# Kernel optimization log

Measured on AMD Instinct MI355X. Metric: run time of the kernel, lower is better.

## Reference

```python
import jax, jax.numpy as jnp
import numpy as np

KNN_K = 5          # neighbor count hard-coded in the original forward (get_entropy(..., k=5))
SAMPLE_K = 256     # self.k: number of tokens sampled per batch item
EPS = 1e-12


def _knn_entropy(x):
    """Per-point k-NN entropy weight: distance to the KNN_K-th nearest neighbor.

    x: [B, N, D] -> [B, N] nonnegative weights (Kozachenko-Leonenko style; the
    per-point entropy contribution is monotone in log d_k, and multinomial
    weights must be nonnegative, so we use d_k itself as the weight).
    """
    B, N, D = x.shape
    sq = jnp.sum(x * x, axis=-1)                                   # [B, N]
    d2 = sq[:, :, None] + sq[:, None, :] - 2.0 * jnp.einsum('bnd,bmd->bnm', x, x)  # [B,N,N]
    d2 = jnp.maximum(d2, 0.0)
    idx = jnp.arange(N)
    d2 = d2.at[:, idx, idx].set(jnp.inf)                           # exclude self
    neg_smallest, _ = jax.lax.top_k(-d2, KNN_K)                    # [B, N, KNN_K]
    dk2 = -neg_smallest[..., -1]                                   # sq dist to k-th NN
    return jnp.sqrt(dk2 + EPS)                                     # [B, N]


def setup_inputs() -> dict:
    key = jax.random.key(0)
    x = jax.random.normal(key, (8, 4096, 256), dtype=jnp.float32)
    return {"x": x}


def reference(x):
    # entropy weights per token (batched; replaces the per-batch numpy loop)
    w = _knn_entropy(x)                                            # [B, N]
    # multinomial sampling WITHOUT replacement via Gumbel top-k trick
    key = jax.random.key(42)
    g = jax.random.gumbel(key, w.shape, dtype=w.dtype)             # [B, N]
    scores = jnp.log(w + EPS) + g
    _, sampled_idx = jax.lax.top_k(scores, SAMPLE_K)               # [B, SAMPLE_K]
    # gather sampled tokens
    sampled = jnp.take_along_axis(x, sampled_idx[:, :, None], axis=1)  # [B, SAMPLE_K, D]
    return (sampled, 0.0)
```

## Files before the change

### kernel.cpp

```cpp
#include <hip/hip_runtime.h>
#include <math.h>
#include <stdint.h>

#define BATCH 8
#define NTOK  4096
#define DIM   256
#define SK    256
#define BQ    128
#define BM    128
#define BK    64
#define MH    2048
#define TOPK  10
#define CANDH 44

typedef __attribute__((ext_vector_type(8))) _Float16 half8;
typedef __attribute__((ext_vector_type(4))) float float4v;
typedef __attribute__((ext_vector_type(16))) float f32x16;

#define GLOAD_LDS16(gp, lp)                                                    \
  __builtin_amdgcn_global_load_lds(                                            \
      (const __attribute__((address_space(1))) unsigned int*)(gp),             \
      (__attribute__((address_space(3))) unsigned int*)(lp), 16, 0, 0)

__device__ __forceinline__ uint32_t umin32(uint32_t a, uint32_t b) { return a < b ? a : b; }
__device__ __forceinline__ uint32_t umax32(uint32_t a, uint32_t b) { return a > b ? a : b; }

__device__ __forceinline__ uint32_t rotl32(uint32_t v, uint32_t r) {
  return (v << r) | (v >> (32u - r));
}
__device__ __forceinline__ void tf_round4(uint32_t& x0, uint32_t& x1,
                                          uint32_t r0, uint32_t r1,
                                          uint32_t r2, uint32_t r3) {
  x0 += x1; x1 = rotl32(x1, r0); x1 ^= x0;
  x0 += x1; x1 = rotl32(x1, r1); x1 ^= x0;
  x0 += x1; x1 = rotl32(x1, r2); x1 ^= x0;
  x0 += x1; x1 = rotl32(x1, r3); x1 ^= x0;
}
__device__ __forceinline__ uint32_t threefry_bits32(uint32_t c_hi, uint32_t c_lo) {
  const uint32_t k0 = 0u, k1 = 42u;
  const uint32_t k2 = k0 ^ k1 ^ 0x1BD11BDAu;
  uint32_t x0 = c_hi + k0;
  uint32_t x1 = c_lo + k1;
  tf_round4(x0, x1, 13u, 15u, 26u, 6u);  x0 += k1; x1 += k2 + 1u;
  tf_round4(x0, x1, 17u, 29u, 16u, 24u); x0 += k2; x1 += k0 + 2u;
  tf_round4(x0, x1, 13u, 15u, 26u, 6u);  x0 += k0; x1 += k1 + 3u;
  tf_round4(x0, x1, 17u, 29u, 16u, 24u); x0 += k1; x1 += k2 + 4u;
  tf_round4(x0, x1, 13u, 15u, 26u, 6u);  x0 += k2; x1 += k0 + 5u;
  return x0 ^ x1;
}

__global__ __launch_bounds__(256) void tofp16_rowsq_kernel(
    const float* __restrict__ x, unsigned short* __restrict__ xh,
    float* __restrict__ sqf) {
  const int row  = blockIdx.x * 4 + (threadIdx.x >> 6);
  const int lane = threadIdx.x & 63;
  const float* xr = x + (size_t)row * DIM;
  double acc = 0.0;
#pragma unroll
  for (int i = 0; i < 4; ++i) {
    const float v = xr[lane + i * 64];
    const _Float16 h = (_Float16)v;
    xh[(size_t)row * DIM + lane + i * 64] = *(const unsigned short*)&h;
    acc += (double)v * (double)v;
  }
#pragma unroll
  for (int off = 32; off > 0; off >>= 1) acc += __shfl_down(acc, off, 64);
  if (lane == 0) sqf[row] = (float)acc;
}

__global__ __launch_bounds__(256, 2) void gemm_knn_kernel(
    const unsigned short* __restrict__ xh, const float* __restrict__ sqf,
    int* __restrict__ cand) {
  __shared__ union {
    unsigned short Bf[2][8192];
    uint32_t M[512][TOPK];
  } U;

  const int wid = (blockIdx.x & 7) * 64 + (blockIdx.x >> 3);
  const int b   = wid >> 6;
  const int qt  = (wid >> 1) & 31;
  const int mh  = wid & 1;
  const int q0  = qt * BQ;
  const int mbase = mh * MH;
  const int t  = threadIdx.x;
  const int w  = t >> 6;
  const int l  = t & 63;
  const int l5 = l & 31;
  const int hi2 = l >> 5;

  const unsigned short* xhb = xh + (size_t)b * NTOK * DIM;
  const float* sqb = sqf + b * NTOK;

  auto stageB = [&](int buf, int m0s, int kb) {
    const int m = m0s + w * 32 + l5;
    const unsigned short* src = xhb + (size_t)m * DIM + kb + hi2 * 8;
#pragma unroll
    for (int c = 0; c < 4; ++c) {
      GLOAD_LDS16(src + c * 16,
                  (char*)&U.Bf[0][0] + buf * 16384 + (c * 4 + w) * 1024 + l * 16);
    }
  };
  stageB(0, mbase, 0);

  const int qg = q0 + w * 32 + l5;
  const unsigned short* qrow = xhb + (size_t)qg * DIM;
  half8 af[16];
#pragma unroll
  for (int kk = 0; kk < 16; ++kk)
    af[kk] = *(const half8*)(qrow + kk * 16 + hi2 * 8);
  const float sqq = sqb[qg];

  __syncthreads();

  uint32_t tv0[TOPK], tv1[TOPK];
#pragma unroll
  for (int j = 0; j < TOPK; ++j) { tv0[j] = 0xFFFFFFFFu; tv1[j] = 0xFFFFFFFFu; }

  for (int mt = 0; mt < MH / BM; ++mt) {
    const int m0 = mbase + mt * BM;
    f32x16 acc[4];
#pragma unroll
    for (int ii = 0; ii < 4; ++ii) acc[ii] = (f32x16)(0.0f);

#pragma unroll
    for (int ks = 0; ks < 4; ++ks) {
      const int s = mt * 4 + ks;
      const int buf = s & 1;
      if (s + 1 < (MH / BM) * 4) {
        const int sn = s + 1;
        stageB(buf ^ 1, mbase + (sn >> 2) * BM, (sn & 3) * BK);
      }
#pragma unroll
      for (int kap = 0; kap < 4; ++kap) {
        const int kk = ks * 4 + kap;
#pragma unroll
        for (int ii = 0; ii < 4; ++ii) {
          const half8 mf = *(const half8*)((const char*)&U.Bf[0][0] +
                                           buf * 16384 + (kap * 4 + ii) * 1024 + l * 16);
          acc[ii] = __builtin_amdgcn_mfma_f32_32x32x16_f16(mf, af[kk], acc[ii], 0, 0, 0);
        }
      }
      __syncthreads();
    }

#pragma unroll
    for (int ii = 0; ii < 4; ++ii) {
      const int mb = m0 + ii * 32 + hi2 * 4;
#pragma unroll
      for (int c = 0; c < 4; ++c) {
        const float4v sqm = *(const float4v*)(sqb + mb + c * 8);
        uint32_t* tv = (c < 2) ? tv0 : tv1;
#pragma unroll
        for (int r = 0; r < 4; ++r) {
          const int mg = mb + c * 8 + r;
          const float d2a = sqq + sqm[r] - 2.0f * acc[ii][c * 4 + r];
          uint32_t v = (__float_as_uint(d2a) & 0xFFFFF000u) | (uint32_t)mg;
          if (v < tv[TOPK - 1]) {
            uint32_t vv = v;
#pragma unroll
            for (int k2 = 0; k2 < TOPK; ++k2) {
              const uint32_t lo = umin32(tv[k2], vv);
              vv = umax32(tv[k2], vv);
              tv[k2] = lo;
            }
          }
        }
      }
    }
  }

  __syncthreads();
  {
    const int base = ((w * 32 + l5) << 2) + (hi2 << 1);
#pragma unroll
    for (int j = 0; j < TOPK; ++j) { U.M[base][j] = tv0[j]; U.M[base + 1][j] = tv1[j]; }
  }
  __syncthreads();
  if (t < BQ) {
    const int q = t;
    const int qglob = q0 + q;
    const int kidx = ((qglob >> 11) == mh) ? 5 : 4;
    uint32_t t6[6];
#pragma unroll
    for (int j = 0; j < 6; ++j) t6[j] = 0xFFFFFFFFu;
    for (int s = 0; s < 4; ++s)
      for (int j = 0; j < 6; ++j) {
        const uint32_t v = U.M[q * 4 + s][j];
        if (v < t6[5]) {
          uint32_t vv = v;
#pragma unroll
          for (int k2 = 0; k2 < 6; ++k2) {
            const uint32_t lo = umin32(t6[k2], vv);
            vv = umax32(t6[k2], vv);
            t6[k2] = lo;
          }
        }
      }
    const float T = __uint_as_float(t6[kidx] & 0xFFFFF000u) + 2.0f;
    int cnt = 0, ov = 0;
    int* cq = cand + (size_t)(b * NTOK + qglob) * (2 * CANDH) + mh * CANDH;
    for (int s = 0; s < 4; ++s) {
      const uint32_t last = U.M[q * 4 + s][TOPK - 1];
      if (__uint_as_float(last & 0xFFFFF000u) < T) ov = 1;
      for (int j = 0; j < TOPK; ++j) {
        const uint32_t v = U.M[q * 4 + s][j];
        if (__uint_as_float(v & 0xFFFFF000u) <= T && cnt < 4 * TOPK)
          cq[1 + cnt++] = (int)(v & 0xFFFu);
      }
    }
    cq[0] = ov ? -1 : cnt;
  }
}

__global__ __launch_bounds__(256) void exact_knn_score_kernel(
    const float* __restrict__ x, const int* __restrict__ cand,
    double* __restrict__ scores) {
  const int qg = blockIdx.x * 4 + (threadIdx.x >> 6);
  const int l  = threadIdx.x & 63;
  const int b  = qg >> 12;
  const int q  = qg & (NTOK - 1);
  const float* xb = x + (size_t)b * NTOK * DIM;
  const int* cq = cand + (size_t)qg * (2 * CANDH);

  double xq[4];
#pragma unroll
  for (int i = 0; i < 4; ++i) xq[i] = (double)xb[(size_t)q * DIM + l + i * 64];

  double t5[5] = {1e300, 1e300, 1e300, 1e300, 1e300};
  auto ins5 = [&](double v) {
    if (v < t5[4]) {
      t5[4] = v;
#pragma unroll
      for (int k2 = 4; k2 > 0; --k2)
        if (t5[k2] < t5[k2 - 1]) { double tmp = t5[k2]; t5[k2] = t5[k2 - 1]; t5[k2 - 1] = tmp; }
    }
  };
  auto process = [&](int m) {
    double acc = 0.0;
#pragma unroll
    for (int i = 0; i < 4; ++i) {
      const double d = xq[i] - (double)xb[(size_t)m * DIM + l + i * 64];
      acc += d * d;
    }
#pragma unroll
    for (int off = 32; off > 0; off >>= 1) acc += __shfl_xor(acc, off, 64);
    ins5(acc);
  };

  for (int h = 0; h < 2; ++h) {
    const int cnt = cq[h * CANDH];
    if (cnt >= 0) {
      for (int c = 0; c < cnt; ++c) {
        const int m = cq[h * CANDH + 1 + c];
        if (m == q) continue;
        process(m);
      }
    } else {
      const int mb2 = h * MH;
      double mv[5] = {1e300, 1e300, 1e300, 1e300, 1e300};
      const float4v* qr4 = (const float4v*)(xb + (size_t)q * DIM);
      for (int it = 0; it < MH / 64; ++it) {
        const int m = mb2 + it * 64 + l;
        if (m == q) continue;
        const float4v* xr4 = (const float4v*)(xb + (size_t)m * DIM);
        double acc = 0.0;
#pragma unroll 16
        for (int d4 = 0; d4 < DIM / 4; ++d4) {
          const float4v qa = qr4[d4];
          const float4v xa = xr4[d4];
#pragma unroll
          for (int j = 0; j < 4; ++j) {
            const double df = (double)qa[j] - (double)xa[j];
            acc += df * df;
          }
        }
        if (acc < mv[4]) {
          mv[4] = acc;
#pragma unroll
          for (int k2 = 4; k2 > 0; --k2)
            if (mv[k2] < mv[k2 - 1]) { double tmp = mv[k2]; mv[k2] = mv[k2 - 1]; mv[k2 - 1] = tmp; }
        }
      }
      int p = 0;
#pragma unroll
      for (int r5 = 0; r5 < 5; ++r5) {
        double best = (p < 5) ? mv[p] : 1e300;
        double mn = best;
#pragma unroll
        for (int off = 32; off > 0; off >>= 1) {
          const double o = __shfl_xor(mn, off, 64);
          mn = (o < mn) ? o : mn;
        }
        const unsigned long long msk = __ballot(best == mn);
        if (l == (int)(__ffsll(msk) - 1)) ++p;
        ins5(mn);
      }
    }
  }

  if (l == 0) {
    const uint32_t bits = threefry_bits32(0u, (uint32_t)qg);
    const uint32_t fb = (bits >> 9) | 0x3F800000u;
    float uf = __uint_as_float(fb) - 1.0f;
    const float tiny = 1.17549435082228750797e-38f;
    uf += tiny;
    if (uf < tiny) uf = tiny;
    const double g = -log(-log((double)uf));
    const double wv = sqrt(t5[4] + 1e-12);
    scores[qg] = log(wv + 1e-12) + g;
  }
}

__global__ __launch_bounds__(1024) void sort_topk_kernel(
    const double* __restrict__ scores, int* __restrict__ sel) {
  __shared__ unsigned long long ko[NTOK];
  __shared__ int ki[NTOK];
  const int b = blockIdx.x;
  const int t = threadIdx.x;
  for (int i = t; i < NTOK; i += 1024) {
    const double s = scores[(size_t)b * NTOK + i];
    unsigned long long u = (unsigned long long)__double_as_longlong(s);
    u = (u & 0x8000000000000000ull) ? ~u : (u | 0x8000000000000000ull);
    ko[i] = u; ki[i] = i;
  }
  __syncthreads();
  for (int k = 2; k <= NTOK; k <<= 1) {
    for (int j = k >> 1; j > 0; j >>= 1) {
      for (int base = 0; base < NTOK; base += 1024) {
        const int i = base + t;
        const int p = i ^ j;
        if (p > i) {
          const bool up = (i & k) == 0;
          unsigned long long a = ko[i], c = ko[p];
          int ia = ki[i], ic = ki[p];
          const bool p_beats = (c > a) || (c == a && ic < ia);
          const bool i_beats = (a > c) || (a == c && ia < ic);
          const bool sw = up ? p_beats : i_beats;
          if (sw) { ko[i] = c; ko[p] = a; ki[i] = ic; ki[p] = ia; }
        }
      }
      __syncthreads();
    }
  }
  if (t < SK) sel[b * SK + t] = ki[t];
}

__global__ __launch_bounds__(256) void gather_kernel(const float* __restrict__ x,
                                                     const int* __restrict__ sel,
                                                     float* __restrict__ out) {
  const int blk = blockIdx.x;
  const int b = blk >> 8;
  const int r = blk & 255;
  const int t = threadIdx.x;
  const int src = sel[b * SK + r];
  out[((size_t)(b * SK + r)) * DIM + t] = x[((size_t)(b * NTOK + src)) * DIM + t];
  if (blk == 0 && t == 0) out[(size_t)BATCH * SK * DIM] = 0.0f;
}

extern "C" void kernel_launch(void* const* d_in, const int* in_sizes, int n_in,
                              void* d_out, int out_size, void* d_ws, size_t ws_size,
                              hipStream_t stream) {
  const float* x = (const float*)d_in[0];
  float* out = (float*)d_out;
  char* ws = (char*)d_ws;

  double* scores  = (double*)(ws + 0);
  float*  sqf     = (float*)(ws + 262144);
  int*    sel     = (int*)(ws + 393216);
  unsigned short* xh = (unsigned short*)(ws + 1048576);
  int*    cand    = (int*)(ws + 17825792);

  tofp16_rowsq_kernel<<<BATCH * NTOK / 4, 256, 0, stream>>>(x, xh, sqf);
  gemm_knn_kernel<<<BATCH * (NTOK / BQ) * 2, 256, 0, stream>>>(xh, sqf, cand);
  exact_knn_score_kernel<<<BATCH * NTOK / 4, 256, 0, stream>>>(x, cand, scores);
  sort_topk_kernel<<<BATCH, 1024, 0, stream>>>(scores, sel);
  gather_kernel<<<BATCH * SK, 256, 0, stream>>>(x, sel, out);
}
```

Measured before the change: 452.6 us.

## Switch kNN GEMM to 16x16x32 MFMA with 512-thread blocks

Rewrites the distance GEMM in the kNN kernel to use 16x16x32 f16 MFMA instructions with 8 waves per block instead of 32x32x16 with 4 waves. The K step per stage is doubled, so there are half as many barrier-separated stages, and the LDS buffers are doubled to hold it. Each lane now keeps a single top-10 list instead of two. The aim is more waves in flight and fewer syncs. The cost is double the LDS use per block and more MFMA instructions.

```diff
diff --git a/kernel.cpp b/kernel.cpp
--- a/kernel.cpp
+++ b/kernel.cpp
@@ -8,14 +8,13 @@
 #define SK    256
 #define BQ    128
 #define BM    128
-#define BK    64
+#define BK    128
 #define MH    2048
 #define TOPK  10
 #define CANDH 44
 
 typedef __attribute__((ext_vector_type(8))) _Float16 half8;
 typedef __attribute__((ext_vector_type(4))) float float4v;
-typedef __attribute__((ext_vector_type(16))) float f32x16;
 
 #define GLOAD_LDS16(gp, lp)                                                    \
   __builtin_amdgcn_global_load_lds(                                            \
@@ -68,11 +67,11 @@
   if (lane == 0) sqf[row] = (float)acc;
 }
 
-__global__ __launch_bounds__(256, 2) void gemm_knn_kernel(
+__global__ __launch_bounds__(512, 4) void gemm_knn_kernel(
     const unsigned short* __restrict__ xh, const float* __restrict__ sqf,
     int* __restrict__ cand) {
   __shared__ union {
-    unsigned short Bf[2][8192];
+    unsigned short Bf[2][16384];
     uint32_t M[512][TOPK];
   } U;
 
@@ -85,84 +84,80 @@
   const int t  = threadIdx.x;
   const int w  = t >> 6;
   const int l  = t & 63;
-  const int l5 = l & 31;
-  const int hi2 = l >> 5;
+  const int lq = l & 15;
+  const int rg = l >> 4;
 
   const unsigned short* xhb = xh + (size_t)b * NTOK * DIM;
   const float* sqb = sqf + b * NTOK;
 
   auto stageB = [&](int buf, int m0s, int kb) {
-    const int m = m0s + w * 32 + l5;
-    const unsigned short* src = xhb + (size_t)m * DIM + kb + hi2 * 8;
+    const int m = m0s + w * 16 + lq;
+    const unsigned short* src = xhb + (size_t)m * DIM + kb + rg * 8;
 #pragma unroll
     for (int c = 0; c < 4; ++c) {
-      GLOAD_LDS16(src + c * 16,
-                  (char*)&U.Bf[0][0] + buf * 16384 + (c * 4 + w) * 1024 + l * 16);
+      GLOAD_LDS16(src + c * 32,
+                  (char*)&U.Bf[0][0] + buf * 32768 + c * 8192 + t * 16);
     }
   };
   stageB(0, mbase, 0);
 
-  const int qg = q0 + w * 32 + l5;
+  const int qg = q0 + w * 16 + lq;
   const unsigned short* qrow = xhb + (size_t)qg * DIM;
-  half8 af[16];
-#pragma unroll
-  for (int kk = 0; kk < 16; ++kk)
-    af[kk] = *(const half8*)(qrow + kk * 16 + hi2 * 8);
+  half8 af[8];
+#pragma unroll
+  for (int kk = 0; kk < 8; ++kk)
+    af[kk] = *(const half8*)(qrow + kk * 32 + rg * 8);
   const float sqq = sqb[qg];
 
   __syncthreads();
 
-  uint32_t tv0[TOPK], tv1[TOPK];
-#pragma unroll
-  for (int j = 0; j < TOPK; ++j) { tv0[j] = 0xFFFFFFFFu; tv1[j] = 0xFFFFFFFFu; }
+  uint32_t tv[TOPK];
+#pragma unroll
+  for (int j = 0; j < TOPK; ++j) tv[j] = 0xFFFFFFFFu;
 
   for (int mt = 0; mt < MH / BM; ++mt) {
     const int m0 = mbase + mt * BM;
-    f32x16 acc[4];
-#pragma unroll
-    for (int ii = 0; ii < 4; ++ii) acc[ii] = (f32x16)(0.0f);
-
-#pragma unroll
-    for (int ks = 0; ks < 4; ++ks) {
-      const int s = mt * 4 + ks;
+    float4v acc[8];
+#pragma unroll
+    for (int ii = 0; ii < 8; ++ii) acc[ii] = (float4v){0.f, 0.f, 0.f, 0.f};
+
+#pragma unroll
+    for (int ks = 0; ks < 2; ++ks) {
+      const int s = mt * 2 + ks;
       const int buf = s & 1;
-      if (s + 1 < (MH / BM) * 4) {
+      if (s + 1 < (MH / BM) * 2) {
         const int sn = s + 1;
-        stageB(buf ^ 1, mbase + (sn >> 2) * BM, (sn & 3) * BK);
-      }
-#pragma unroll
-      for (int kap = 0; kap < 4; ++kap) {
-        const int kk = ks * 4 + kap;
-#pragma unroll
-        for (int ii = 0; ii < 4; ++ii) {
+        stageB(buf ^ 1, mbase + (sn >> 1) * BM, (sn & 1) * BK);
+      }
+#pragma unroll
+      for (int kc = 0; kc < 4; ++kc) {
+        const int kk = ks * 4 + kc;
+#pragma unroll
+        for (int ii = 0; ii < 8; ++ii) {
           const half8 mf = *(const half8*)((const char*)&U.Bf[0][0] +
-                                           buf * 16384 + (kap * 4 + ii) * 1024 + l * 16);
-          acc[ii] = __builtin_amdgcn_mfma_f32_32x32x16_f16(mf, af[kk], acc[ii], 0, 0, 0);
+                                           buf * 32768 + (kc * 8 + ii) * 1024 + l * 16);
+          acc[ii] = __builtin_amdgcn_mfma_f32_16x16x32_f16(mf, af[kk], acc[ii], 0, 0, 0);
         }
       }
       __syncthreads();
     }
 
 #pragma unroll
-    for (int ii = 0; ii < 4; ++ii) {
-      const int mb = m0 + ii * 32 + hi2 * 4;
-#pragma unroll
-      for (int c = 0; c < 4; ++c) {
-        const float4v sqm = *(const float4v*)(sqb + mb + c * 8);
-        uint32_t* tv = (c < 2) ? tv0 : tv1;
-#pragma unroll
-        for (int r = 0; r < 4; ++r) {
-          const int mg = mb + c * 8 + r;
-          const float d2a = sqq + sqm[r] - 2.0f * acc[ii][c * 4 + r];
-          uint32_t v = (__float_as_uint(d2a) & 0xFFFFF000u) | (uint32_t)mg;
-          if (v < tv[TOPK - 1]) {
-            uint32_t vv = v;
-#pragma unroll
-            for (int k2 = 0; k2 < TOPK; ++k2) {
-              const uint32_t lo = umin32(tv[k2], vv);
-              vv = umax32(tv[k2], vv);
-              tv[k2] = lo;
-            }
+    for (int ii = 0; ii < 8; ++ii) {
+      const int mb = m0 + ii * 16 + rg * 4;
+      const float4v sqm = *(const float4v*)(sqb + mb);
+#pragma unroll
+      for (int r = 0; r < 4; ++r) {
+        const int mg = mb + r;
+        const float d2a = sqq + sqm[r] - 2.0f * acc[ii][r];
+        const uint32_t v = (__float_as_uint(d2a) & 0xFFFFF000u) | (uint32_t)mg;
+        if (v < tv[TOPK - 1]) {
+          uint32_t vv = v;
+#pragma unroll
+          for (int k2 = 0; k2 < TOPK; ++k2) {
+            const uint32_t lo = umin32(tv[k2], vv);
+            vv = umax32(tv[k2], vv);
+            tv[k2] = lo;
           }
         }
       }
@@ -171,9 +166,9 @@
 
   __syncthreads();
   {
-    const int base = ((w * 32 + l5) << 2) + (hi2 << 1);
-#pragma unroll
-    for (int j = 0; j < TOPK; ++j) { U.M[base][j] = tv0[j]; U.M[base + 1][j] = tv1[j]; }
+    const int slotM = ((w * 16 + lq) << 2) + rg;
+#pragma unroll
+    for (int j = 0; j < TOPK; ++j) U.M[slotM][j] = tv[j];
   }
   __syncthreads();
   if (t < BQ) {
@@ -371,7 +366,7 @@
   int*    cand    = (int*)(ws + 17825792);
 
   tofp16_rowsq_kernel<<<BATCH * NTOK / 4, 256, 0, stream>>>(x, xh, sqf);
-  gemm_knn_kernel<<<BATCH * (NTOK / BQ) * 2, 256, 0, stream>>>(xh, sqf, cand);
+  gemm_knn_kernel<<<BATCH * (NTOK / BQ) * 2, 512, 0, stream>>>(xh, sqf, cand);
   exact_knn_score_kernel<<<BATCH * NTOK / 4, 256, 0, stream>>>(x, cand, scores);
   sort_topk_kernel<<<BATCH, 1024, 0, stream>>>(scores, sel);
   gather_kernel<<<BATCH * SK, 256, 0, stream>>>(x, sel, out);
```

After: 511.9 us. +13.1%, slower.

## Halve query tile and split waves across query and key dimensions

Applied to the files above, without the earlier changes.

Reduces the query tile from 128 to 64 rows and arranges the four waves as a 2x2 grid: two query groups by two key-column groups. Each wave now keeps two MFMA accumulators and one top-k list instead of four accumulators and two lists. This lowers register pressure so launch bounds can request 4 blocks per CU, and it doubles the grid size. The trade-off is that each staged B tile is reused across fewer queries, so every key tile is loaded twice as often overall.

```diff
diff --git a/kernel.cpp b/kernel.cpp
--- a/kernel.cpp
+++ b/kernel.cpp
@@ -6,7 +6,7 @@
 #define NTOK  4096
 #define DIM   256
 #define SK    256
-#define BQ    128
+#define BQ    64
 #define BM    128
 #define BK    64
 #define MH    2048
@@ -68,22 +68,24 @@
   if (lane == 0) sqf[row] = (float)acc;
 }
 
-__global__ __launch_bounds__(256, 2) void gemm_knn_kernel(
+__global__ __launch_bounds__(256, 4) void gemm_knn_kernel(
     const unsigned short* __restrict__ xh, const float* __restrict__ sqf,
     int* __restrict__ cand) {
   __shared__ union {
     unsigned short Bf[2][8192];
-    uint32_t M[512][TOPK];
+    uint32_t M[256][TOPK];
   } U;
 
-  const int wid = (blockIdx.x & 7) * 64 + (blockIdx.x >> 3);
-  const int b   = wid >> 6;
-  const int qt  = (wid >> 1) & 31;
+  const int wid = (blockIdx.x & 7) * 128 + (blockIdx.x >> 3);
+  const int b   = wid >> 7;
+  const int qt  = (wid >> 1) & 63;
   const int mh  = wid & 1;
   const int q0  = qt * BQ;
   const int mbase = mh * MH;
   const int t  = threadIdx.x;
   const int w  = t >> 6;
+  const int wq = w & 1;
+  const int wm = w >> 1;
   const int l  = t & 63;
   const int l5 = l & 31;
   const int hi2 = l >> 5;
@@ -102,7 +104,7 @@
   };
   stageB(0, mbase, 0);
 
-  const int qg = q0 + w * 32 + l5;
+  const int qg = q0 + wq * 32 + l5;
   const unsigned short* qrow = xhb + (size_t)qg * DIM;
   half8 af[16];
 #pragma unroll
@@ -112,15 +114,15 @@
 
   __syncthreads();
 
-  uint32_t tv0[TOPK], tv1[TOPK];
-#pragma unroll
-  for (int j = 0; j < TOPK; ++j) { tv0[j] = 0xFFFFFFFFu; tv1[j] = 0xFFFFFFFFu; }
+  uint32_t tv[TOPK];
+#pragma unroll
+  for (int j = 0; j < TOPK; ++j) tv[j] = 0xFFFFFFFFu;
 
   for (int mt = 0; mt < MH / BM; ++mt) {
     const int m0 = mbase + mt * BM;
-    f32x16 acc[4];
-#pragma unroll
-    for (int ii = 0; ii < 4; ++ii) acc[ii] = (f32x16)(0.0f);
+    f32x16 acc[2];
+    acc[0] = (f32x16)(0.0f);
+    acc[1] = (f32x16)(0.0f);
 
 #pragma unroll
     for (int ks = 0; ks < 4; ++ks) {
@@ -134,27 +136,27 @@
       for (int kap = 0; kap < 4; ++kap) {
         const int kk = ks * 4 + kap;
 #pragma unroll
-        for (int ii = 0; ii < 4; ++ii) {
+        for (int iw = 0; iw < 2; ++iw) {
+          const int g = kap * 4 + wm * 2 + iw;
           const half8 mf = *(const half8*)((const char*)&U.Bf[0][0] +
-                                           buf * 16384 + (kap * 4 + ii) * 1024 + l * 16);
-          acc[ii] = __builtin_amdgcn_mfma_f32_32x32x16_f16(mf, af[kk], acc[ii], 0, 0, 0);
+                                           buf * 16384 + g * 1024 + l * 16);
+          acc[iw] = __builtin_amdgcn_mfma_f32_32x32x16_f16(mf, af[kk], acc[iw], 0, 0, 0);
         }
       }
       __syncthreads();
     }
 
 #pragma unroll
-    for (int ii = 0; ii < 4; ++ii) {
-      const int mb = m0 + ii * 32 + hi2 * 4;
+    for (int iw = 0; iw < 2; ++iw) {
+      const int mb = m0 + (wm * 2 + iw) * 32 + hi2 * 4;
 #pragma unroll
       for (int c = 0; c < 4; ++c) {
         const float4v sqm = *(const float4v*)(sqb + mb + c * 8);
-        uint32_t* tv = (c < 2) ? tv0 : tv1;
 #pragma unroll
         for (int r = 0; r < 4; ++r) {
           const int mg = mb + c * 8 + r;
-          const float d2a = sqq + sqm[r] - 2.0f * acc[ii][c * 4 + r];
-          uint32_t v = (__float_as_uint(d2a) & 0xFFFFF000u) | (uint32_t)mg;
+          const float d2a = sqq + sqm[r] - 2.0f * acc[iw][c * 4 + r];
+          const uint32_t v = (__float_as_uint(d2a) & 0xFFFFF000u) | (uint32_t)mg;
           if (v < tv[TOPK - 1]) {
             uint32_t vv = v;
 #pragma unroll
@@ -171,9 +173,9 @@
 
   __syncthreads();
   {
-    const int base = ((w * 32 + l5) << 2) + (hi2 << 1);
-#pragma unroll
-    for (int j = 0; j < TOPK; ++j) { U.M[base][j] = tv0[j]; U.M[base + 1][j] = tv1[j]; }
+    const int slotM = ((wq * 32 + l5) << 2) + (wm << 1) + hi2;
+#pragma unroll
+    for (int j = 0; j < TOPK; ++j) U.M[slotM][j] = tv[j];
   }
   __syncthreads();
   if (t < BQ) {
```

Result: slower. 466.6 us (+3.1%).
